# Optimization experiments

Measured on AMD Instinct MI355X. Metric: run time of the kernel, lower is better.

Reference implementation:

```python
import jax, jax.numpy as jnp
import numpy as np

B, S, IN, H, Q, M, K = 32, 2048, 128, 256, 16, 64, 3


def setup_inputs() -> dict:
    key = jax.random.key(0)
    ks = jax.random.split(key, 12)
    rn = lambda k, shp, s=0.05: (jax.random.normal(k, shp, jnp.float32) * s)
    return {
        "input_sequence": rn(ks[0], (B, S, IN), 1.0),
        "W_ih0": rn(ks[1], (4 * H, IN)),
        "W_hh0": rn(ks[2], (4 * H, H)),
        "b_ih0": jnp.zeros((4 * H,), jnp.float32),
        "b_hh0": jnp.zeros((4 * H,), jnp.float32),
        "W_ih1": rn(ks[3], (4 * H, H)),
        "W_hh1": rn(ks[4], (4 * H, H)),
        "b_ih1": jnp.zeros((4 * H,), jnp.float32),
        "b_hh1": jnp.zeros((4 * H,), jnp.float32),
        "W_cq": rn(ks[5], (Q, H)),
        "b_cq": jnp.zeros((Q,), jnp.float32),
        "mem_keys": rn(ks[6], (M, Q), 1.0),
        "mem_vals": rn(ks[7], (M, H), 1.0),
        "W_out": rn(ks[8], (H, 2 * H)),
        "b_out": jnp.zeros((H,), jnp.float32),
        "classical_weight": jnp.float32(0.7),
        "quantum_weight": jnp.float32(0.3),
    }


def _lstm_layer(x, W_ih, W_hh, b_ih, b_hh):
    """PyTorch-convention LSTM layer (gate order i,f,g,o), batch_first input."""
    Bb = x.shape[0]
    Hh = W_hh.shape[1]
    # precompute the input contribution for all timesteps: [B,S,4H]
    xg = jnp.einsum('bsi,gi->bsg', x, W_ih) + b_ih + b_hh

    def step(carry, xt):
        h, c = carry
        g = xt + h @ W_hh.T  # [B,4H]
        i, f, gg, o = jnp.split(g, 4, axis=-1)
        i = jax.nn.sigmoid(i)
        f = jax.nn.sigmoid(f)
        gg = jnp.tanh(gg)
        o = jax.nn.sigmoid(o)
        c = f * c + i * gg
        h = o * jnp.tanh(c)
        return (h, c), h

    init = (jnp.zeros((Bb, Hh), x.dtype), jnp.zeros((Bb, Hh), x.dtype))
    _, hs = jax.lax.scan(step, init, jnp.swapaxes(xg, 0, 1))  # [S,B,H]
    return jnp.swapaxes(hs, 0, 1)


def _forward(input_sequence, W_ih0, W_hh0, b_ih0, b_hh0, W_ih1, W_hh1, b_ih1,
             b_hh1, W_cq, b_cq, mem_keys, mem_vals, W_out, b_out,
             classical_weight, quantum_weight):
    # classical 2-layer LSTM
    h1 = _lstm_layer(input_sequence, W_ih0, W_hh0, b_ih0, b_hh0)
    lstm_out = _lstm_layer(h1, W_ih1, W_hh1, b_ih1, b_hh1)  # [B,S,H]

    # classical_to_quantum + tanh -> per-token query [B,S,Q]
    q = jnp.tanh(jnp.einsum('bsh,qh->bsq', lstm_out, W_cq) + b_cq)

    # batched k-NN read over the quantum memory (cosine similarity, k=3)
    eps = jnp.float32(1e-8)
    qn = q / (jnp.linalg.norm(q, axis=-1, keepdims=True) + eps)
    kn = mem_keys / (jnp.linalg.norm(mem_keys, axis=-1, keepdims=True) + eps)
    sims = jnp.einsum('bsq,mq->bsm', qn, kn)          # [B,S,M]
    top_vals, top_idx = jax.lax.top_k(sims, K)        # [B,S,K]
    gathered = mem_vals[top_idx]                      # [B,S,K,H]

    # similarity-weighted average of retrieved contents
    tot = jnp.sum(top_vals, axis=-1, keepdims=True)   # [B,S,1]
    weighted = jnp.einsum('bsk,bskh->bsh', top_vals, gathered)
    enhanced = jnp.where(tot > 0, weighted / jnp.where(tot == 0, 1.0, tot), 0.0)

    # combine streams and project
    combined = jnp.concatenate(
        [classical_weight * lstm_out, quantum_weight * enhanced], axis=-1)
    out = jnp.einsum('bsc,hc->bsh', combined, W_out) + b_out  # [B,S,H]
    return out


def reference(input_sequence, W_ih0, W_hh0, b_ih0, b_hh0, W_ih1, W_hh1, b_ih1,
              b_hh1, W_cq, b_cq, mem_keys, mem_vals, W_out, b_out,
              classical_weight, quantum_weight):
    return _forward(input_sequence, W_ih0, W_hh0, b_ih0, b_hh0, W_ih1, W_hh1,
                    b_ih1, b_hh1, W_cq, b_cq, mem_keys, mem_vals, W_out, b_out,
                    classical_weight, quantum_weight)
```

## Files before the change

kernel.cpp:

```cpp
#include <hip/hip_runtime.h>
#include <cstdint>
#include <cstddef>
#include <math.h>

#define B_   32
#define S_   2048
#define IN_  128
#define H_   256
#define Q_   16
#define M_   64
#define D_   4

typedef unsigned long long u64;
typedef __attribute__((ext_vector_type(4))) unsigned int u32x4;

__device__ __forceinline__ float4 ld4(const float* p) { return *(const float4*)p; }

#define AGLD64(p)    __hip_atomic_load((p),  __ATOMIC_RELAXED, __HIP_MEMORY_SCOPE_AGENT)
#define AGST64(p, v) __hip_atomic_store((p), (v), __ATOMIC_RELAXED, __HIP_MEMORY_SCOPE_AGENT)

__device__ __forceinline__ u32x4 mall_load_2x64(const u64* p) {
  u32x4 q;
  asm volatile("global_load_dwordx4 %0, %1, off sc0 sc1\n\ts_waitcnt vmcnt(0)"
               : "=v"(q) : "v"(p) : "memory");
  return q;
}

__device__ __forceinline__ float sigm_f(float x) { return 1.0f / (1.0f + __expf(-x)); }
__device__ __forceinline__ float tanh_f(float x) { return 1.0f - 2.0f / (__expf(2.0f * x) + 1.0f); }

__global__ __launch_bounds__(256, 1) void lstm2(
    const float* __restrict__ x,
    const float* __restrict__ Wih0, const float* __restrict__ bih0,
    const float* __restrict__ bhh0, const float* __restrict__ Whh0,
    const float* __restrict__ Wih1, const float* __restrict__ bih1,
    const float* __restrict__ bhh1, const float* __restrict__ Whh1,
    float* __restrict__ out,
    u64* __restrict__ exs)
{
  const int f = blockIdx.x;
  const int n = f >> 5;
  const int b = f & 31;

  const int tid = threadIdx.x;
  const int w   = tid >> 6;
  const int l   = tid & 63;
  const int kc  = l & 7;
  const int rg  = l >> 3;
  const int wrg = w * 8 + rg;
  const int col = n * 32 + wrg;

  __shared__ float w1[128][257];
  __shared__ float aring[8][256];
  __shared__ float hring[2][256];
  __shared__ float x_sh[2][IN_];

#pragma unroll
  for (int s2 = 0; s2 < 8; s2++) aring[s2][tid] = 0.0f;
  hring[0][tid] = 0.0f;
  hring[1][tid] = 0.0f;

  float4 wf0[4][8], wf1[4][8], wi0[4][4];
  float rb0[4], rb1[4];
#pragma unroll
  for (int g = 0; g < 4; g++) {
    const int row = g * 256 + col;
    const float* p0 = Whh0 + (size_t)row * 256 + 4 * kc;
    const float* p1 = Whh1 + (size_t)row * 256 + 4 * kc;
    const float* pi = Wih0 + (size_t)row * 128 + 4 * kc;
#pragma unroll
    for (int j = 0; j < 8; j++) {
      wf0[g][j] = ld4(p0 + 32 * j);
      wf1[g][j] = ld4(p1 + 32 * j);
    }
#pragma unroll
    for (int j = 0; j < 4; j++) wi0[g][j] = ld4(pi + 32 * j);
    rb0[g] = bih0[row] + bhh0[row];
    rb1[g] = bih1[row] + bhh1[row];
    const float* pw = Wih1 + (size_t)row * 256 + 4 * kc;
    float* dst = &w1[g * 32 + wrg][4 * kc];
#pragma unroll
    for (int j = 0; j < 8; j++) *(float4*)(dst + 32 * j) = ld4(pw + 32 * j);
  }

  const float* xrow = x + (size_t)b * S_ * IN_;
  float* outp = out + (size_t)b * S_ * H_;
  u64* sexb = exs + (size_t)b * 1024;

  if (tid < IN_) {
    x_sh[0][tid] = xrow[tid];
    x_sh[1][tid] = xrow[IN_ + tid];
  }
  float xreg = (tid < IN_) ? xrow[(size_t)2 * IN_ + tid] : 0.0f;
  float cst0 = 0.0f, cst1 = 0.0f;
  float xa0s[4], xa1s[4] = {0, 0, 0, 0};
  __syncthreads();

  {
    const float* xb = x_sh[0];
    float4 xv[4];
#pragma unroll
    for (int j = 0; j < 4; j++) xv[j] = ld4(xb + 4 * kc + 32 * j);
#pragma unroll
    for (int g = 0; g < 4; g++) {
      float4 s4 = {0, 0, 0, 0};
#pragma unroll
      for (int j = 0; j < 4; j++) {
        s4.x += wi0[g][j].x * xv[j].x; s4.y += wi0[g][j].y * xv[j].y;
        s4.z += wi0[g][j].z * xv[j].z; s4.w += wi0[g][j].w * xv[j].w;
      }
      float s = (s4.x + s4.y) + (s4.z + s4.w);
      s += __shfl_xor(s, 1); s += __shfl_xor(s, 2); s += __shfl_xor(s, 4);
      xa0s[g] = s + rb0[g];
    }
  }

  bool dead = false;
  for (int t = 0; t < S_ + D_; ++t) {
    const bool doA = (t < S_);
    const int  u   = t - D_;
    const bool doH = (u >= 0);
    const int  pa = t & 1, ph = u & 1;
    const unsigned eA = (unsigned)(t + 1), eH = (unsigned)(u + 1);

    float xreg_n = 0.0f;
    if (tid < IN_ && t + 2 < S_) {
      int tn = (t + 3 < S_) ? t + 3 : S_ - 1;
      xreg_n = xrow[(size_t)tn * IN_ + tid];
    }

    if (doA) {
      const float* ap = aring[(t - 1) & 7];
      float4 av[8];
#pragma unroll
      for (int j = 0; j < 8; j++) av[j] = ld4(ap + 4 * kc + 32 * j);
      float gv[4];
#pragma unroll
      for (int g = 0; g < 4; g++) {
        float4 s4 = {0, 0, 0, 0};
#pragma unroll
        for (int j = 0; j < 8; j++) {
          s4.x += wf0[g][j].x * av[j].x; s4.y += wf0[g][j].y * av[j].y;
          s4.z += wf0[g][j].z * av[j].z; s4.w += wf0[g][j].w * av[j].w;
        }
        float s = (s4.x + s4.y) + (s4.z + s4.w);
        s += __shfl_xor(s, 1); s += __shfl_xor(s, 2); s += __shfl_xor(s, 4);
        gv[g] = s + xa0s[g];
      }
      float ig = sigm_f(gv[0]);
      float fg = sigm_f(gv[1]);
      float cg = tanh_f(gv[2]);
      float og = sigm_f(gv[3]);
      cst0 = fg * cst0 + ig * cg;
      float a = og * tanh_f(cst0);
      if (kc == 0) {
        u64 pk = ((u64)eA << 32) | (u64)__float_as_uint(a);
        AGST64(sexb + ((0 * 2 + pa) << 8) + col, pk);
        aring[t & 7][col] = a;
      }
    }
    if (doH) {
      const float* hp = hring[(t - 1) & 1];
      float4 hv[8];
#pragma unroll
      for (int j = 0; j < 8; j++) hv[j] = ld4(hp + 4 * kc + 32 * j);
      float gv[4];
#pragma unroll
      for (int g = 0; g < 4; g++) {
        float4 s4 = {0, 0, 0, 0};
#pragma unroll
        for (int j = 0; j < 8; j++) {
          s4.x += wf1[g][j].x * hv[j].x; s4.y += wf1[g][j].y * hv[j].y;
          s4.z += wf1[g][j].z * hv[j].z; s4.w += wf1[g][j].w * hv[j].w;
        }
        float s = (s4.x + s4.y) + (s4.z + s4.w);
        s += __shfl_xor(s, 1); s += __shfl_xor(s, 2); s += __shfl_xor(s, 4);
        gv[g] = s + xa1s[g];
      }
      float ig = sigm_f(gv[0]);
      float fg = sigm_f(gv[1]);
      float cg = tanh_f(gv[2]);
      float og = sigm_f(gv[3]);
      cst1 = fg * cst1 + ig * cg;
      float h = og * tanh_f(cst1);
      if (kc == 0) {
        outp[(size_t)u * H_ + col] = h;
        u64 pk = ((u64)eH << 32) | (u64)__float_as_uint(h);
        AGST64(sexb + ((1 * 2 + ph) << 8) + col, pk);
        hring[u & 1][col] = h;
      }
    }

    if (t + 1 < S_) {
      const float* xb = x_sh[(t + 1) & 1];
      float4 xv[4];
#pragma unroll
      for (int j = 0; j < 4; j++) xv[j] = ld4(xb + 4 * kc + 32 * j);
#pragma unroll
      for (int g = 0; g < 4; g++) {
        float4 s4 = {0, 0, 0, 0};
#pragma unroll
        for (int j = 0; j < 4; j++) {
          s4.x += wi0[g][j].x * xv[j].x; s4.y += wi0[g][j].y * xv[j].y;
          s4.z += wi0[g][j].z * xv[j].z; s4.w += wi0[g][j].w * xv[j].w;
        }
        float s = (s4.x + s4.y) + (s4.z + s4.w);
        s += __shfl_xor(s, 1); s += __shfl_xor(s, 2); s += __shfl_xor(s, 4);
        xa0s[g] = s + rb0[g];
      }
    }
    {
      const int v = t - D_ + 1;
      if (v >= 0 && v < S_) {
        const float* avp = aring[v & 7];
        float4 av[8];
#pragma unroll
        for (int j = 0; j < 8; j++) av[j] = ld4(avp + 4 * kc + 32 * j);
#pragma unroll
        for (int g = 0; g < 4; g++) {
          const float* wr = &w1[g * 32 + wrg][4 * kc];
          float4 s4 = {0, 0, 0, 0};
#pragma unroll
          for (int j = 0; j < 8; j++) {
            float4 wv = ld4(wr + 32 * j);
            s4.x += wv.x * av[j].x; s4.y += wv.y * av[j].y;
            s4.z += wv.z * av[j].z; s4.w += wv.w * av[j].w;
          }
          float s = (s4.x + s4.y) + (s4.z + s4.w);
          s += __shfl_xor(s, 1); s += __shfl_xor(s, 2); s += __shfl_xor(s, 4);
          xa1s[g] = s + rb1[g];
        }
      }
    }

    {
      const bool isA = (tid < 128);
      const int  pi2 = isA ? tid : tid - 128;
      const bool ownp = ((pi2 >> 4) == n);
      const bool act  = isA ? doA : doH;
      bool need = act && !ownp && !dead;
      if (need) {
        const unsigned etag = isA ? eA : eH;
        const int plane = isA ? (0 * 2 + pa) : (1 * 2 + ph);
        u64* base = sexb + (plane << 8) + 2 * pi2;
        unsigned val0 = 0, val1 = 0;
        bool got = false;
#pragma unroll 1
        for (int it = 0; it < 16 && !got; ++it) {
          u32x4 q = mall_load_2x64(base);
          if (q.y == etag && q.w == etag) { val0 = q.x; val1 = q.z; got = true; }
        }
        if (!got) {
          bool g0 = false, g1 = false;
          unsigned guard = 0;
          while (!(g0 && g1)) {
            if (!g0) { u64 v = AGLD64(base);     if ((unsigned)(v >> 32) == etag) { val0 = (unsigned)v; g0 = true; } }
            if (!g1) { u64 v = AGLD64(base + 1); if ((unsigned)(v >> 32) == etag) { val1 = (unsigned)v; g1 = true; } }
            if (++guard >= (1u << 20)) { dead = true; break; }
          }
        }
        float2 f2;
        f2.x = __uint_as_float(val0);
        f2.y = __uint_as_float(val1);
        if (isA) *(float2*)&aring[t & 7][2 * pi2] = f2;
        else     *(float2*)&hring[u & 1][2 * pi2] = f2;
      }
    }

    if (tid < IN_ && t < S_) x_sh[t & 1][tid] = xreg;
    xreg = xreg_n;
    __syncthreads();
  }
}

__global__ __launch_bounds__(256) void knn_enh(
    const float* __restrict__ lstm, const float* __restrict__ Wcq,
    const float* __restrict__ bcq, const float* __restrict__ keys,
    const float* __restrict__ vals, const float* __restrict__ qwp,
    float* __restrict__ enh)
{
  const int tid  = threadIdx.x;
  const int wave = tid >> 6, lane = tid & 63;
  const int t = blockIdx.x * 4 + wave;

  __shared__ float xsh[4][256];
  __shared__ float qsh[4][16];

  const float* xrow = lstm + (size_t)t * H_;
  float4 x4 = ld4(xrow + lane * 4);
  *(float4*)&xsh[wave][lane * 4] = x4;
  __syncthreads();

  const int j = lane & 15, seg = lane >> 4;
  const float* wrow = Wcq + j * H_ + seg * 64;
  const float* xseg = &xsh[wave][seg * 64];
  float p = 0.0f;
#pragma unroll
  for (int c = 0; c < 64; c += 4) {
    float4 w4 = ld4(wrow + c);
    p += w4.x * xseg[c] + w4.y * xseg[c + 1] + w4.z * xseg[c + 2] + w4.w * xseg[c + 3];
  }
  p += __shfl_xor(p, 16);
  p += __shfl_xor(p, 32);
  float q = tanhf(p + bcq[j]);

  float sq = q * q;
  sq += __shfl_xor(sq, 1); sq += __shfl_xor(sq, 2);
  sq += __shfl_xor(sq, 4); sq += __shfl_xor(sq, 8);
  float qn = q / (sqrtf(sq) + 1e-8f);
  if (lane < 16) qsh[wave][lane] = qn;
  __syncthreads();

  const int m = lane;
  const float* krow = keys + m * Q_;
  float kv[16]; float kn2 = 0.0f;
#pragma unroll
  for (int jj = 0; jj < 16; jj++) { kv[jj] = krow[jj]; kn2 += kv[jj] * kv[jj]; }
  float rn = 1.0f / (sqrtf(kn2) + 1e-8f);
  float sim = 0.0f;
#pragma unroll
  for (int jj = 0; jj < 16; jj++) sim += qsh[wave][jj] * kv[jj];
  sim *= rn;

  float rem = sim;
  float tv[3]; int ti[3];
#pragma unroll
  for (int k = 0; k < 3; k++) {
    float v = rem; int idx = m;
#pragma unroll
    for (int d = 1; d < 64; d <<= 1) {
      float ov = __shfl_xor(v, d);
      int   oi = __shfl_xor(idx, d);
      if (ov > v || (ov == v && oi < idx)) { v = ov; idx = oi; }
    }
    tv[k] = v; ti[k] = idx;
    if (m == idx) rem = -INFINITY;
  }
  float tot = tv[0] + tv[1] + tv[2];

  float ex = 0, ey = 0, ez = 0, ew = 0;
#pragma unroll
  for (int k = 0; k < 3; k++) {
    float4 vv = ld4(vals + (size_t)ti[k] * H_ + lane * 4);
    ex += tv[k] * vv.x; ey += tv[k] * vv.y;
    ez += tv[k] * vv.z; ew += tv[k] * vv.w;
  }
  float inv = (tot > 0.0f) ? 1.0f / tot : 0.0f;
  const float qw = qwp[0];

  float4 o;
  o.x = qw * ex * inv; o.y = qw * ey * inv;
  o.z = qw * ez * inv; o.w = qw * ew * inv;
  *(float4*)&enh[(size_t)t * H_ + lane * 4] = o;
}

__global__ __launch_bounds__(256) void gemm_cat(
    float* __restrict__ io, const float* __restrict__ A2,
    const float* __restrict__ Bw, const float* __restrict__ bias,
    const float* __restrict__ cwp)
{
  __shared__ float As[16][68];
  __shared__ float Bs[16][260];
  const int tid  = threadIdx.x;
  const int row0 = blockIdx.x * 64;
  const int tx = tid & 15, ty = tid >> 4;
  const int lr = tid >> 2;
  const int lk = (tid & 3) << 2;
  const float cw = cwp[0];

  float acc[4][16];
#pragma unroll
  for (int i = 0; i < 4; i++)
#pragma unroll
    for (int j = 0; j < 16; j++) acc[i][j] = 0.0f;

  for (int k0 = 0; k0 < 512; k0 += 16) {
    float4 av;
    if (k0 < 256) {
      av = ld4(io + (size_t)(row0 + lr) * 256 + k0 + lk);
      av.x *= cw; av.y *= cw; av.z *= cw; av.w *= cw;
    } else {
      av = ld4(A2 + (size_t)(row0 + lr) * 256 + (k0 - 256) + lk);
    }
    As[lk + 0][lr] = av.x; As[lk + 1][lr] = av.y;
    As[lk + 2][lr] = av.z; As[lk + 3][lr] = av.w;
    const float* bp = Bw + (size_t)tid * 512 + k0;
#pragma unroll
    for (int q = 0; q < 4; q++) {
      float4 b4 = ld4(bp + 4 * q);
      Bs[4 * q + 0][tid] = b4.x; Bs[4 * q + 1][tid] = b4.y;
      Bs[4 * q + 2][tid] = b4.z; Bs[4 * q + 3][tid] = b4.w;
    }
    __syncthreads();
#pragma unroll
    for (int k = 0; k < 16; k++) {
      float4 a4 = *(const float4*)&As[k][ty << 2];
      float aa[4] = {a4.x, a4.y, a4.z, a4.w};
#pragma unroll
      for (int cc = 0; cc < 4; cc++) {
        float4 b4 = *(const float4*)&Bs[k][cc * 64 + (tx << 2)];
        float bb[4] = {b4.x, b4.y, b4.z, b4.w};
#pragma unroll
        for (int i = 0; i < 4; i++)
#pragma unroll
          for (int jj = 0; jj < 4; jj++) acc[i][cc * 4 + jj] += aa[i] * bb[jj];
      }
    }
    __syncthreads();
  }

#pragma unroll
  for (int i = 0; i < 4; i++) {
#pragma unroll
    for (int cc = 0; cc < 4; cc++) {
      int c0 = cc * 64 + (tx << 2);
      float4 o;
      o.x = acc[i][cc * 4 + 0] + bias[c0 + 0];
      o.y = acc[i][cc * 4 + 1] + bias[c0 + 1];
      o.z = acc[i][cc * 4 + 2] + bias[c0 + 2];
      o.w = acc[i][cc * 4 + 3] + bias[c0 + 3];
      *(float4*)&io[(size_t)(row0 + (ty << 2) + i) * 256 + c0] = o;
    }
  }
}

extern "C" void kernel_launch(void* const* d_in, const int* in_sizes, int n_in,
                              void* d_out, int out_size, void* d_ws, size_t ws_size,
                              hipStream_t stream)
{
  const float* x    = (const float*)d_in[0];
  const float* Wih0 = (const float*)d_in[1];
  const float* Whh0 = (const float*)d_in[2];
  const float* bih0 = (const float*)d_in[3];
  const float* bhh0 = (const float*)d_in[4];
  const float* Wih1 = (const float*)d_in[5];
  const float* Whh1 = (const float*)d_in[6];
  const float* bih1 = (const float*)d_in[7];
  const float* bhh1 = (const float*)d_in[8];
  const float* Wcq  = (const float*)d_in[9];
  const float* bcq  = (const float*)d_in[10];
  const float* keys = (const float*)d_in[11];
  const float* vals = (const float*)d_in[12];
  const float* Wout = (const float*)d_in[13];
  const float* bout = (const float*)d_in[14];
  const float* cw   = (const float*)d_in[15];
  const float* qw   = (const float*)d_in[16];
  float* out = (float*)d_out;

  const size_t HE = (size_t)B_ * S_ * H_;
  if (ws_size < HE * sizeof(float)) return;
  u64* exs = (u64*)d_ws;
  float* enh = (float*)d_ws;

  const int MT = B_ * S_;
  dim3 blk(256);

  hipMemsetAsync(exs, 0, (size_t)32 * 1024 * sizeof(u64), stream);
  lstm2<<<dim3(256), blk, 0, stream>>>(x, Wih0, bih0, bhh0, Whh0,
                                       Wih1, bih1, bhh1, Whh1, out, exs);

  knn_enh<<<dim3(MT / 4), blk, 0, stream>>>(out, Wcq, bcq, keys, vals, qw, enh);

  gemm_cat<<<dim3(MT / 64), blk, 0, stream>>>(out, enh, Wout, bout, cw);
}
```

Measured before the change: 13.57 ms.

## Process four batch rows per LSTM block and batch cross-block exchange loads

Each persistent LSTM block now handles four batch rows for its 32-column slice, which cuts the grid from 256 to 64 blocks. The register-resident weights are reused across the rows, and the four rows' peer-exchange polls are issued together as one batched set of MALL loads. The aim is to amortise per-step synchronisation and exchange latency over more work per step. In exchange, each block does roughly four times the serial compute per timestep, so per-step latency may rise. Register pressure also grows with the per-row state arrays.

Result: slower. 33.91 ms (+149.9%).

```diff
diff --git a/kernel.cpp b/kernel.cpp
--- a/kernel.cpp
+++ b/kernel.cpp
@@ -10,6 +10,7 @@
 #define Q_   16
 #define M_   64
 #define D_   4
+#define R_   4
 
 typedef unsigned long long u64;
 typedef __attribute__((ext_vector_type(4))) unsigned int u32x4;
@@ -24,6 +25,20 @@
   asm volatile("global_load_dwordx4 %0, %1, off sc0 sc1\n\ts_waitcnt vmcnt(0)"
                : "=v"(q) : "v"(p) : "memory");
   return q;
+}
+__device__ __forceinline__ void mall_load4(const u64* p0, const u64* p1,
+                                           const u64* p2, const u64* p3,
+                                           u32x4& q0, u32x4& q1,
+                                           u32x4& q2, u32x4& q3) {
+  asm volatile(
+      "global_load_dwordx4 %0, %4, off sc0 sc1\n\t"
+      "global_load_dwordx4 %1, %5, off sc0 sc1\n\t"
+      "global_load_dwordx4 %2, %6, off sc0 sc1\n\t"
+      "global_load_dwordx4 %3, %7, off sc0 sc1\n\t"
+      "s_waitcnt vmcnt(0)"
+      : "=&v"(q0), "=&v"(q1), "=&v"(q2), "=&v"(q3)
+      : "v"(p0), "v"(p1), "v"(p2), "v"(p3)
+      : "memory");
 }
 
 __device__ __forceinline__ float sigm_f(float x) { return 1.0f / (1.0f + __expf(-x)); }
@@ -38,9 +53,9 @@
     float* __restrict__ out,
     u64* __restrict__ exs)
 {
-  const int f = blockIdx.x;
-  const int n = f >> 5;
-  const int b = f & 31;
+  const int f  = blockIdx.x;
+  const int n  = f & 7;
+  const int r0 = (f >> 3) * R_;
 
   const int tid = threadIdx.x;
   const int w   = tid >> 6;
@@ -51,14 +66,12 @@
   const int col = n * 32 + wrg;
 
   __shared__ float w1[128][257];
-  __shared__ float aring[8][256];
-  __shared__ float hring[2][256];
-  __shared__ float x_sh[2][IN_];
-
-#pragma unroll
-  for (int s2 = 0; s2 < 8; s2++) aring[s2][tid] = 0.0f;
-  hring[0][tid] = 0.0f;
-  hring[1][tid] = 0.0f;
+  __shared__ float aring[4][R_][256];
+  __shared__ float hring[2][R_][256];
+  __shared__ float x_sh[2][R_][IN_];
+
+  for (int i = tid; i < 4 * R_ * 256; i += 256) ((float*)aring)[i] = 0.0f;
+  for (int i = tid; i < 2 * R_ * 256; i += 256) ((float*)hring)[i] = 0.0f;
 
   float4 wf0[4][8], wf1[4][8], wi0[4][4];
   float rb0[4], rb1[4];
@@ -83,21 +96,25 @@
     for (int j = 0; j < 8; j++) *(float4*)(dst + 32 * j) = ld4(pw + 32 * j);
   }
 
-  const float* xrow = x + (size_t)b * S_ * IN_;
-  float* outp = out + (size_t)b * S_ * H_;
-  u64* sexb = exs + (size_t)b * 1024;
-
-  if (tid < IN_) {
-    x_sh[0][tid] = xrow[tid];
-    x_sh[1][tid] = xrow[IN_ + tid];
-  }
-  float xreg = (tid < IN_) ? xrow[(size_t)2 * IN_ + tid] : 0.0f;
-  float cst0 = 0.0f, cst1 = 0.0f;
-  float xa0s[4], xa1s[4] = {0, 0, 0, 0};
+  const int xrr = tid >> 6, xe = (tid & 63) * 2;
+  const float* xrow_t = x + (size_t)(r0 + xrr) * S_ * IN_ + xe;
+  *(float2*)&x_sh[0][xrr][xe] = *(const float2*)(xrow_t);
+  *(float2*)&x_sh[1][xrr][xe] = *(const float2*)(xrow_t + IN_);
+  float2 xreg = *(const float2*)(xrow_t + 2 * IN_);
+
+  float cst0[R_], cst1[R_];
+  float xa0s[R_][4], xa1s[R_][4];
+#pragma unroll
+  for (int rr = 0; rr < R_; rr++) {
+    cst0[rr] = 0.0f; cst1[rr] = 0.0f;
+#pragma unroll
+    for (int g = 0; g < 4; g++) xa1s[rr][g] = 0.0f;
+  }
   __syncthreads();
 
-  {
-    const float* xb = x_sh[0];
+#pragma unroll
+  for (int rr = 0; rr < R_; rr++) {
+    const float* xb = x_sh[0][rr];
     float4 xv[4];
 #pragma unroll
     for (int j = 0; j < 4; j++) xv[j] = ld4(xb + 4 * kc + 32 * j);
@@ -111,7 +128,7 @@
       }
       float s = (s4.x + s4.y) + (s4.z + s4.w);
       s += __shfl_xor(s, 1); s += __shfl_xor(s, 2); s += __shfl_xor(s, 4);
-      xa0s[g] = s + rb0[g];
+      xa0s[rr][g] = s + rb0[g];
     }
   }
 
@@ -123,151 +140,173 @@
     const int  pa = t & 1, ph = u & 1;
     const unsigned eA = (unsigned)(t + 1), eH = (unsigned)(u + 1);
 
-    float xreg_n = 0.0f;
-    if (tid < IN_ && t + 2 < S_) {
+    float2 xreg_n = {0.0f, 0.0f};
+    if (t + 2 < S_) {
       int tn = (t + 3 < S_) ? t + 3 : S_ - 1;
-      xreg_n = xrow[(size_t)tn * IN_ + tid];
+      xreg_n = *(const float2*)(xrow_t + (size_t)tn * IN_);
     }
 
     if (doA) {
-      const float* ap = aring[(t - 1) & 7];
-      float4 av[8];
-#pragma unroll
-      for (int j = 0; j < 8; j++) av[j] = ld4(ap + 4 * kc + 32 * j);
-      float gv[4];
-#pragma unroll
-      for (int g = 0; g < 4; g++) {
-        float4 s4 = {0, 0, 0, 0};
-#pragma unroll
-        for (int j = 0; j < 8; j++) {
-          s4.x += wf0[g][j].x * av[j].x; s4.y += wf0[g][j].y * av[j].y;
-          s4.z += wf0[g][j].z * av[j].z; s4.w += wf0[g][j].w * av[j].w;
-        }
-        float s = (s4.x + s4.y) + (s4.z + s4.w);
-        s += __shfl_xor(s, 1); s += __shfl_xor(s, 2); s += __shfl_xor(s, 4);
-        gv[g] = s + xa0s[g];
-      }
-      float ig = sigm_f(gv[0]);
-      float fg = sigm_f(gv[1]);
-      float cg = tanh_f(gv[2]);
-      float og = sigm_f(gv[3]);
-      cst0 = fg * cst0 + ig * cg;
-      float a = og * tanh_f(cst0);
-      if (kc == 0) {
-        u64 pk = ((u64)eA << 32) | (u64)__float_as_uint(a);
-        AGST64(sexb + ((0 * 2 + pa) << 8) + col, pk);
-        aring[t & 7][col] = a;
+#pragma unroll
+      for (int rr = 0; rr < R_; rr++) {
+        const float* ap = aring[(t - 1) & 3][rr];
+        float4 av[8];
+#pragma unroll
+        for (int j = 0; j < 8; j++) av[j] = ld4(ap + 4 * kc + 32 * j);
+        float gv[4];
+#pragma unroll
+        for (int g = 0; g < 4; g++) {
+          float4 s4 = {0, 0, 0, 0};
+#pragma unroll
+          for (int j = 0; j < 8; j++) {
+            s4.x += wf0[g][j].x * av[j].x; s4.y += wf0[g][j].y * av[j].y;
+            s4.z += wf0[g][j].z * av[j].z; s4.w += wf0[g][j].w * av[j].w;
+          }
+          float s = (s4.x + s4.y) + (s4.z + s4.w);
+          s += __shfl_xor(s, 1); s += __shfl_xor(s, 2); s += __shfl_xor(s, 4);
+          gv[g] = s + xa0s[rr][g];
+        }
+        float ig = sigm_f(gv[0]);
+        float fg = sigm_f(gv[1]);
+        float cg = tanh_f(gv[2]);
+        float og = sigm_f(gv[3]);
+        cst0[rr] = fg * cst0[rr] + ig * cg;
+        float a = og * tanh_f(cst0[rr]);
+        if (kc == 0) {
+          u64 pk = ((u64)eA << 32) | (u64)__float_as_uint(a);
+          AGST64(exs + (size_t)(r0 + rr) * 1024 + ((0 * 2 + pa) << 8) + col, pk);
+          aring[t & 3][rr][col] = a;
+        }
       }
     }
     if (doH) {
-      const float* hp = hring[(t - 1) & 1];
-      float4 hv[8];
-#pragma unroll
-      for (int j = 0; j < 8; j++) hv[j] = ld4(hp + 4 * kc + 32 * j);
-      float gv[4];
-#pragma unroll
-      for (int g = 0; g < 4; g++) {
-        float4 s4 = {0, 0, 0, 0};
-#pragma unroll
-        for (int j = 0; j < 8; j++) {
-          s4.x += wf1[g][j].x * hv[j].x; s4.y += wf1[g][j].y * hv[j].y;
-          s4.z += wf1[g][j].z * hv[j].z; s4.w += wf1[g][j].w * hv[j].w;
-        }
-        float s = (s4.x + s4.y) + (s4.z + s4.w);
-        s += __shfl_xor(s, 1); s += __shfl_xor(s, 2); s += __shfl_xor(s, 4);
-        gv[g] = s + xa1s[g];
-      }
-      float ig = sigm_f(gv[0]);
-      float fg = sigm_f(gv[1]);
-      float cg = tanh_f(gv[2]);
-      float og = sigm_f(gv[3]);
-      cst1 = fg * cst1 + ig * cg;
-      float h = og * tanh_f(cst1);
-      if (kc == 0) {
-        outp[(size_t)u * H_ + col] = h;
-        u64 pk = ((u64)eH << 32) | (u64)__float_as_uint(h);
-        AGST64(sexb + ((1 * 2 + ph) << 8) + col, pk);
-        hring[u & 1][col] = h;
+#pragma unroll
+      for (int rr = 0; rr < R_; rr++) {
+        const float* hp = hring[(t - 1) & 1][rr];
+        float4 hv[8];
+#pragma unroll
+        for (int j = 0; j < 8; j++) hv[j] = ld4(hp + 4 * kc + 32 * j);
+        float gv[4];
+#pragma unroll
+        for (int g = 0; g < 4; g++) {
+          float4 s4 = {0, 0, 0, 0};
+#pragma unroll
+          for (int j = 0; j < 8; j++) {
+            s4.x += wf1[g][j].x * hv[j].x; s4.y += wf1[g][j].y * hv[j].y;
+            s4.z += wf1[g][j].z * hv[j].z; s4.w += wf1[g][j].w * hv[j].w;
+          }
+          float s = (s4.x + s4.y) + (s4.z + s4.w);
+          s += __shfl_xor(s, 1); s += __shfl_xor(s, 2); s += __shfl_xor(s, 4);
+          gv[g] = s + xa1s[rr][g];
+        }
+        float ig = sigm_f(gv[0]);
+        float fg = sigm_f(gv[1]);
+        float cg = tanh_f(gv[2]);
+        float og = sigm_f(gv[3]);
+        cst1[rr] = fg * cst1[rr] + ig * cg;
+        float h = og * tanh_f(cst1[rr]);
+        if (kc == 0) {
+          u64 pk = ((u64)eH << 32) | (u64)__float_as_uint(h);
+          AGST64(exs + (size_t)(r0 + rr) * 1024 + ((1 * 2 + ph) << 8) + col, pk);
+          out[((size_t)(r0 + rr) * S_ + u) * H_ + col] = h;
+          hring[u & 1][rr][col] = h;
+        }
       }
     }
 
     if (t + 1 < S_) {
-      const float* xb = x_sh[(t + 1) & 1];
-      float4 xv[4];
-#pragma unroll
-      for (int j = 0; j < 4; j++) xv[j] = ld4(xb + 4 * kc + 32 * j);
-#pragma unroll
-      for (int g = 0; g < 4; g++) {
-        float4 s4 = {0, 0, 0, 0};
-#pragma unroll
-        for (int j = 0; j < 4; j++) {
-          s4.x += wi0[g][j].x * xv[j].x; s4.y += wi0[g][j].y * xv[j].y;
-          s4.z += wi0[g][j].z * xv[j].z; s4.w += wi0[g][j].w * xv[j].w;
-        }
-        float s = (s4.x + s4.y) + (s4.z + s4.w);
-        s += __shfl_xor(s, 1); s += __shfl_xor(s, 2); s += __shfl_xor(s, 4);
-        xa0s[g] = s + rb0[g];
+#pragma unroll
+      for (int rr = 0; rr < R_; rr++) {
+        const float* xb = x_sh[(t + 1) & 1][rr];
+        float4 xv[4];
+#pragma unroll
+        for (int j = 0; j < 4; j++) xv[j] = ld4(xb + 4 * kc + 32 * j);
+#pragma unroll
+        for (int g = 0; g < 4; g++) {
+          float4 s4 = {0, 0, 0, 0};
+#pragma unroll
+          for (int j = 0; j < 4; j++) {
+            s4.x += wi0[g][j].x * xv[j].x; s4.y += wi0[g][j].y * xv[j].y;
+            s4.z += wi0[g][j].z * xv[j].z; s4.w += wi0[g][j].w * xv[j].w;
+          }
+          float s = (s4.x + s4.y) + (s4.z + s4.w);
+          s += __shfl_xor(s, 1); s += __shfl_xor(s, 2); s += __shfl_xor(s, 4);
+          xa0s[rr][g] = s + rb0[g];
+        }
       }
     }
     {
       const int v = t - D_ + 1;
       if (v >= 0 && v < S_) {
-        const float* avp = aring[v & 7];
-        float4 av[8];
-#pragma unroll
-        for (int j = 0; j < 8; j++) av[j] = ld4(avp + 4 * kc + 32 * j);
-#pragma unroll
-        for (int g = 0; g < 4; g++) {
-          const float* wr = &w1[g * 32 + wrg][4 * kc];
-          float4 s4 = {0, 0, 0, 0};
-#pragma unroll
-          for (int j = 0; j < 8; j++) {
-            float4 wv = ld4(wr + 32 * j);
-            s4.x += wv.x * av[j].x; s4.y += wv.y * av[j].y;
-            s4.z += wv.z * av[j].z; s4.w += wv.w * av[j].w;
+#pragma unroll
+        for (int rr = 0; rr < R_; rr++) {
+          const float* avp = aring[v & 3][rr];
+          float4 av[8];
+#pragma unroll
+          for (int j = 0; j < 8; j++) av[j] = ld4(avp + 4 * kc + 32 * j);
+#pragma unroll
+          for (int g = 0; g < 4; g++) {
+            const float* wr = &w1[g * 32 + wrg][4 * kc];
+            float4 s4 = {0, 0, 0, 0};
+#pragma unroll
+            for (int j = 0; j < 8; j++) {
+              float4 wv = ld4(wr + 32 * j);
+              s4.x += wv.x * av[j].x; s4.y += wv.y * av[j].y;
+              s4.z += wv.z * av[j].z; s4.w += wv.w * av[j].w;
+            }
+            float s = (s4.x + s4.y) + (s4.z + s4.w);
+            s += __shfl_xor(s, 1); s += __shfl_xor(s, 2); s += __shfl_xor(s, 4);
+            xa1s[rr][g] = s + rb1[g];
           }
-          float s = (s4.x + s4.y) + (s4.z + s4.w);
-          s += __shfl_xor(s, 1); s += __shfl_xor(s, 2); s += __shfl_xor(s, 4);
-          xa1s[g] = s + rb1[g];
         }
       }
     }
 
     {
       const bool isA = (tid < 128);
-      const int  pi2 = isA ? tid : tid - 128;
+      const int  pi2 = tid & 127;
       const bool ownp = ((pi2 >> 4) == n);
       const bool act  = isA ? doA : doH;
-      bool need = act && !ownp && !dead;
-      if (need) {
+      if (act && !ownp && !dead) {
         const unsigned etag = isA ? eA : eH;
         const int plane = isA ? (0 * 2 + pa) : (1 * 2 + ph);
-        u64* base = sexb + (plane << 8) + 2 * pi2;
-        unsigned val0 = 0, val1 = 0;
-        bool got = false;
+        u64* base0 = exs + (size_t)(r0 + 0) * 1024 + (plane << 8) + 2 * pi2;
+        u64* base1 = base0 + 1024;
+        u64* base2 = base0 + 2048;
+        u64* base3 = base0 + 3072;
+        u32x4 q0, q1, q2, q3;
+        mall_load4(base0, base1, base2, base3, q0, q1, q2, q3);
+        u32x4 qs[R_] = {q0, q1, q2, q3};
+        u64* bases[R_] = {base0, base1, base2, base3};
+#pragma unroll
+        for (int rr = 0; rr < R_; rr++) {
+          u32x4 q = qs[rr];
+          bool got = (q.y == etag && q.w == etag);
 #pragma unroll 1
-        for (int it = 0; it < 16 && !got; ++it) {
-          u32x4 q = mall_load_2x64(base);
-          if (q.y == etag && q.w == etag) { val0 = q.x; val1 = q.z; got = true; }
-        }
-        if (!got) {
-          bool g0 = false, g1 = false;
-          unsigned guard = 0;
-          while (!(g0 && g1)) {
-            if (!g0) { u64 v = AGLD64(base);     if ((unsigned)(v >> 32) == etag) { val0 = (unsigned)v; g0 = true; } }
-            if (!g1) { u64 v = AGLD64(base + 1); if ((unsigned)(v >> 32) == etag) { val1 = (unsigned)v; g1 = true; } }
-            if (++guard >= (1u << 20)) { dead = true; break; }
+          for (int it = 0; it < 16 && !got; ++it) {
+            q = mall_load_2x64(bases[rr]);
+            got = (q.y == etag && q.w == etag);
           }
-        }
-        float2 f2;
-        f2.x = __uint_as_float(val0);
-        f2.y = __uint_as_float(val1);
-        if (isA) *(float2*)&aring[t & 7][2 * pi2] = f2;
-        else     *(float2*)&hring[u & 1][2 * pi2] = f2;
-      }
-    }
-
-    if (tid < IN_ && t < S_) x_sh[t & 1][tid] = xreg;
+          unsigned val0 = q.x, val1 = q.z;
+          if (!got) {
+            bool g0 = false, g1 = false;
+            unsigned guard = 0;
+            while (!(g0 && g1)) {
+              if (!g0) { u64 v2 = AGLD64(bases[rr]);     if ((unsigned)(v2 >> 32) == etag) { val0 = (unsigned)v2; g0 = true; } }
+              if (!g1) { u64 v2 = AGLD64(bases[rr] + 1); if ((unsigned)(v2 >> 32) == etag) { val1 = (unsigned)v2; g1 = true; } }
+              if (++guard >= (1u << 20)) { dead = true; break; }
+            }
+          }
+          float2 f2;
+          f2.x = __uint_as_float(val0);
+          f2.y = __uint_as_float(val1);
+          if (isA) *(float2*)&aring[t & 3][rr][2 * pi2] = f2;
+          else     *(float2*)&hring[u & 1][rr][2 * pi2] = f2;
+        }
+      }
+    }
+
+    if (t < S_) *(float2*)&x_sh[t & 1][xrr][xe] = xreg;
     xreg = xreg_n;
     __syncthreads();
   }
@@ -456,8 +495,8 @@
   dim3 blk(256);
 
   hipMemsetAsync(exs, 0, (size_t)32 * 1024 * sizeof(u64), stream);
-  lstm2<<<dim3(256), blk, 0, stream>>>(x, Wih0, bih0, bhh0, Whh0,
-                                       Wih1, bih1, bhh1, Whh1, out, exs);
+  lstm2<<<dim3(64), blk, 0, stream>>>(x, Wih0, bih0, bhh0, Whh0,
+                                      Wih1, bih1, bhh1, Whh1, out, exs);
 
   knn_enh<<<dim3(MT / 4), blk, 0, stream>>>(out, Wcq, bcq, keys, vals, qw, enh);
 
```

## Process two batch rows per LSTM block, halving grid and overlapping exchange loads

Applied to the files above, without the earlier changes.

Each persistent LSTM block now handles two batch rows instead of one, so the register-resident recurrent weights are reused across rows and the grid shrinks from 256 to 128 blocks. The cross-block exchange now issues both rows' MALL loads before the input-projection work and waits on them afterwards, hiding part of the polling latency. The aring ring is reduced to 4 slots per row to fit the extra LDS. The trade-off is roughly double the serial compute per block per timestep, which may lengthen the critical path of the recurrence.

New measurement: 23.44 ms. +72.7%, slower.

```diff
diff --git a/kernel.cpp b/kernel.cpp
--- a/kernel.cpp
+++ b/kernel.cpp
@@ -10,6 +10,7 @@
 #define Q_   16
 #define M_   64
 #define D_   4
+#define R_   2
 
 typedef unsigned long long u64;
 typedef __attribute__((ext_vector_type(4))) unsigned int u32x4;
@@ -24,6 +25,15 @@
   asm volatile("global_load_dwordx4 %0, %1, off sc0 sc1\n\ts_waitcnt vmcnt(0)"
                : "=v"(q) : "v"(p) : "memory");
   return q;
+}
+__device__ __forceinline__ void mall_issue2(const u64* p0, const u64* p1,
+                                            u32x4& q0, u32x4& q1) {
+  asm volatile("global_load_dwordx4 %0, %2, off sc0 sc1\n\t"
+               "global_load_dwordx4 %1, %3, off sc0 sc1"
+               : "=&v"(q0), "=&v"(q1) : "v"(p0), "v"(p1) : "memory");
+}
+__device__ __forceinline__ void mall_wait2(u32x4& q0, u32x4& q1) {
+  asm volatile("s_waitcnt vmcnt(0)" : "+v"(q0), "+v"(q1) :: "memory");
 }
 
 __device__ __forceinline__ float sigm_f(float x) { return 1.0f / (1.0f + __expf(-x)); }
@@ -38,9 +48,9 @@
     float* __restrict__ out,
     u64* __restrict__ exs)
 {
-  const int f = blockIdx.x;
-  const int n = f >> 5;
-  const int b = f & 31;
+  const int f  = blockIdx.x;
+  const int n  = f & 7;
+  const int r0 = (f >> 3) * R_;
 
   const int tid = threadIdx.x;
   const int w   = tid >> 6;
@@ -51,14 +61,12 @@
   const int col = n * 32 + wrg;
 
   __shared__ float w1[128][257];
-  __shared__ float aring[8][256];
-  __shared__ float hring[2][256];
-  __shared__ float x_sh[2][IN_];
-
-#pragma unroll
-  for (int s2 = 0; s2 < 8; s2++) aring[s2][tid] = 0.0f;
-  hring[0][tid] = 0.0f;
-  hring[1][tid] = 0.0f;
+  __shared__ float aring[4][R_][256];
+  __shared__ float hring[2][R_][256];
+  __shared__ float x_sh[2][R_][IN_];
+
+  for (int i = tid; i < 4 * R_ * 256; i += 256) ((float*)aring)[i] = 0.0f;
+  for (int i = tid; i < 2 * R_ * 256; i += 256) ((float*)hring)[i] = 0.0f;
 
   float4 wf0[4][8], wf1[4][8], wi0[4][4];
   float rb0[4], rb1[4];
@@ -83,37 +91,96 @@
     for (int j = 0; j < 8; j++) *(float4*)(dst + 32 * j) = ld4(pw + 32 * j);
   }
 
-  const float* xrow = x + (size_t)b * S_ * IN_;
-  float* outp = out + (size_t)b * S_ * H_;
-  u64* sexb = exs + (size_t)b * 1024;
-
-  if (tid < IN_) {
-    x_sh[0][tid] = xrow[tid];
-    x_sh[1][tid] = xrow[IN_ + tid];
-  }
-  float xreg = (tid < IN_) ? xrow[(size_t)2 * IN_ + tid] : 0.0f;
-  float cst0 = 0.0f, cst1 = 0.0f;
-  float xa0s[4], xa1s[4] = {0, 0, 0, 0};
+  const int xrr = tid >> 7, xe = tid & 127;
+  const float* xrow_t = x + (size_t)(r0 + xrr) * S_ * IN_ + xe;
+  x_sh[0][xrr][xe] = xrow_t[0];
+  x_sh[1][xrr][xe] = xrow_t[IN_];
+  float xreg = xrow_t[2 * IN_];
+
+  float cst0_0 = 0.0f, cst0_1 = 0.0f, cst1_0 = 0.0f, cst1_1 = 0.0f;
+  float xa0s_0[4], xa0s_1[4];
+  float xa1s_0[4] = {0, 0, 0, 0}, xa1s_1[4] = {0, 0, 0, 0};
   __syncthreads();
 
-  {
-    const float* xb = x_sh[0];
-    float4 xv[4];
-#pragma unroll
-    for (int j = 0; j < 4; j++) xv[j] = ld4(xb + 4 * kc + 32 * j);
-#pragma unroll
-    for (int g = 0; g < 4; g++) {
-      float4 s4 = {0, 0, 0, 0};
-#pragma unroll
-      for (int j = 0; j < 4; j++) {
-        s4.x += wi0[g][j].x * xv[j].x; s4.y += wi0[g][j].y * xv[j].y;
-        s4.z += wi0[g][j].z * xv[j].z; s4.w += wi0[g][j].w * xv[j].w;
-      }
-      float s = (s4.x + s4.y) + (s4.z + s4.w);
-      s += __shfl_xor(s, 1); s += __shfl_xor(s, 2); s += __shfl_xor(s, 4);
-      xa0s[g] = s + rb0[g];
-    }
-  }
+#define XA0_ROW(RR, BUF)                                                     \
+  { const float* xb = x_sh[BUF][RR];                                         \
+    float4 xv[4];                                                            \
+    _Pragma("unroll") for (int j = 0; j < 4; j++)                            \
+      xv[j] = ld4(xb + 4 * kc + 32 * j);                                     \
+    _Pragma("unroll") for (int g = 0; g < 4; g++) {                          \
+      float4 s4 = {0, 0, 0, 0};                                              \
+      _Pragma("unroll") for (int j = 0; j < 4; j++) {                        \
+        s4.x += wi0[g][j].x * xv[j].x; s4.y += wi0[g][j].y * xv[j].y;        \
+        s4.z += wi0[g][j].z * xv[j].z; s4.w += wi0[g][j].w * xv[j].w; }      \
+      float s = (s4.x + s4.y) + (s4.z + s4.w);                               \
+      s += __shfl_xor(s, 1); s += __shfl_xor(s, 2); s += __shfl_xor(s, 4);   \
+      xa0s_##RR[g] = s + rb0[g]; } }
+
+#define L0_ROW(RR)                                                           \
+  { const float* ap = aring[(t - 1) & 3][RR];                                \
+    float4 av[8];                                                            \
+    _Pragma("unroll") for (int j = 0; j < 8; j++)                            \
+      av[j] = ld4(ap + 4 * kc + 32 * j);                                     \
+    float gv[4];                                                             \
+    _Pragma("unroll") for (int g = 0; g < 4; g++) {                          \
+      float4 s4 = {0, 0, 0, 0};                                              \
+      _Pragma("unroll") for (int j = 0; j < 8; j++) {                        \
+        s4.x += wf0[g][j].x * av[j].x; s4.y += wf0[g][j].y * av[j].y;        \
+        s4.z += wf0[g][j].z * av[j].z; s4.w += wf0[g][j].w * av[j].w; }      \
+      float s = (s4.x + s4.y) + (s4.z + s4.w);                               \
+      s += __shfl_xor(s, 1); s += __shfl_xor(s, 2); s += __shfl_xor(s, 4);   \
+      gv[g] = s + xa0s_##RR[g]; }                                            \
+    float ig = sigm_f(gv[0]), fg = sigm_f(gv[1]);                            \
+    float cg = tanh_f(gv[2]), og = sigm_f(gv[3]);                            \
+    cst0_##RR = fg * cst0_##RR + ig * cg;                                    \
+    float a = og * tanh_f(cst0_##RR);                                        \
+    if (kc == 0) {                                                           \
+      u64 pk = ((u64)eA << 32) | (u64)__float_as_uint(a);                    \
+      AGST64(exs + (size_t)(r0 + RR) * 1024 + (pa << 8) + col, pk);          \
+      aring[t & 3][RR][col] = a; } }
+
+#define L1_ROW(RR)                                                           \
+  { const float* hp = hring[(t - 1) & 1][RR];                                \
+    float4 hv[8];                                                            \
+    _Pragma("unroll") for (int j = 0; j < 8; j++)                            \
+      hv[j] = ld4(hp + 4 * kc + 32 * j);                                     \
+    float gv[4];                                                             \
+    _Pragma("unroll") for (int g = 0; g < 4; g++) {                          \
+      float4 s4 = {0, 0, 0, 0};                                              \
+      _Pragma("unroll") for (int j = 0; j < 8; j++) {                        \
+        s4.x += wf1[g][j].x * hv[j].x; s4.y += wf1[g][j].y * hv[j].y;        \
+        s4.z += wf1[g][j].z * hv[j].z; s4.w += wf1[g][j].w * hv[j].w; }      \
+      float s = (s4.x + s4.y) + (s4.z + s4.w);                               \
+      s += __shfl_xor(s, 1); s += __shfl_xor(s, 2); s += __shfl_xor(s, 4);   \
+      gv[g] = s + xa1s_##RR[g]; }                                            \
+    float ig = sigm_f(gv[0]), fg = sigm_f(gv[1]);                            \
+    float cg = tanh_f(gv[2]), og = sigm_f(gv[3]);                            \
+    cst1_##RR = fg * cst1_##RR + ig * cg;                                    \
+    float h = og * tanh_f(cst1_##RR);                                        \
+    if (kc == 0) {                                                           \
+      u64 pk = ((u64)eH << 32) | (u64)__float_as_uint(h);                    \
+      AGST64(exs + (size_t)(r0 + RR) * 1024 + ((2 + ph) << 8) + col, pk);    \
+      out[((size_t)(r0 + RR) * S_ + u) * H_ + col] = h;                      \
+      hring[u & 1][RR][col] = h; } }
+
+#define XA1_ROW(RR)                                                          \
+  { const float* avp = aring[v & 3][RR];                                     \
+    float4 av[8];                                                            \
+    _Pragma("unroll") for (int j = 0; j < 8; j++)                            \
+      av[j] = ld4(avp + 4 * kc + 32 * j);                                    \
+    _Pragma("unroll") for (int g = 0; g < 4; g++) {                          \
+      const float* wr = &w1[g * 32 + wrg][4 * kc];                           \
+      float4 s4 = {0, 0, 0, 0};                                              \
+      _Pragma("unroll") for (int j = 0; j < 8; j++) {                        \
+        float4 wv = ld4(wr + 32 * j);                                        \
+        s4.x += wv.x * av[j].x; s4.y += wv.y * av[j].y;                      \
+        s4.z += wv.z * av[j].z; s4.w += wv.w * av[j].w; }                    \
+      float s = (s4.x + s4.y) + (s4.z + s4.w);                               \
+      s += __shfl_xor(s, 1); s += __shfl_xor(s, 2); s += __shfl_xor(s, 4);   \
+      xa1s_##RR[g] = s + rb1[g]; } }
+
+  XA0_ROW(0, 0)
+  XA0_ROW(1, 0)
 
   bool dead = false;
   for (int t = 0; t < S_ + D_; ++t) {
@@ -124,153 +191,83 @@
     const unsigned eA = (unsigned)(t + 1), eH = (unsigned)(u + 1);
 
     float xreg_n = 0.0f;
-    if (tid < IN_ && t + 2 < S_) {
+    if (t + 2 < S_) {
       int tn = (t + 3 < S_) ? t + 3 : S_ - 1;
-      xreg_n = xrow[(size_t)tn * IN_ + tid];
-    }
-
-    if (doA) {
-      const float* ap = aring[(t - 1) & 7];
-      float4 av[8];
-#pragma unroll
-      for (int j = 0; j < 8; j++) av[j] = ld4(ap + 4 * kc + 32 * j);
-      float gv[4];
-#pragma unroll
-      for (int g = 0; g < 4; g++) {
-        float4 s4 = {0, 0, 0, 0};
-#pragma unroll
-        for (int j = 0; j < 8; j++) {
-          s4.x += wf0[g][j].x * av[j].x; s4.y += wf0[g][j].y * av[j].y;
-          s4.z += wf0[g][j].z * av[j].z; s4.w += wf0[g][j].w * av[j].w;
-        }
-        float s = (s4.x + s4.y) + (s4.z + s4.w);
-        s += __shfl_xor(s, 1); s += __shfl_xor(s, 2); s += __shfl_xor(s, 4);
-        gv[g] = s + xa0s[g];
-      }
-      float ig = sigm_f(gv[0]);
-      float fg = sigm_f(gv[1]);
-      float cg = tanh_f(gv[2]);
-      float og = sigm_f(gv[3]);
-      cst0 = fg * cst0 + ig * cg;
-      float a = og * tanh_f(cst0);
-      if (kc == 0) {
-        u64 pk = ((u64)eA << 32) | (u64)__float_as_uint(a);
-        AGST64(sexb + ((0 * 2 + pa) << 8) + col, pk);
-        aring[t & 7][col] = a;
-      }
-    }
-    if (doH) {
-      const float* hp = hring[(t - 1) & 1];
-      float4 hv[8];
-#pragma unroll
-      for (int j = 0; j < 8; j++) hv[j] = ld4(hp + 4 * kc + 32 * j);
-      float gv[4];
-#pragma unroll
-      for (int g = 0; g < 4; g++) {
-        float4 s4 = {0, 0, 0, 0};
-#pragma unroll
-        for (int j = 0; j < 8; j++) {
-          s4.x += wf1[g][j].x * hv[j].x; s4.y += wf1[g][j].y * hv[j].y;
-          s4.z += wf1[g][j].z * hv[j].z; s4.w += wf1[g][j].w * hv[j].w;
-        }
-        float s = (s4.x + s4.y) + (s4.z + s4.w);
-        s += __shfl_xor(s, 1); s += __shfl_xor(s, 2); s += __shfl_xor(s, 4);
-        gv[g] = s + xa1s[g];
-      }
-      float ig = sigm_f(gv[0]);
-      float fg = sigm_f(gv[1]);
-      float cg = tanh_f(gv[2]);
-      float og = sigm_f(gv[3]);
-      cst1 = fg * cst1 + ig * cg;
-      float h = og * tanh_f(cst1);
-      if (kc == 0) {
-        outp[(size_t)u * H_ + col] = h;
-        u64 pk = ((u64)eH << 32) | (u64)__float_as_uint(h);
-        AGST64(sexb + ((1 * 2 + ph) << 8) + col, pk);
-        hring[u & 1][col] = h;
-      }
-    }
+      xreg_n = xrow_t[(size_t)tn * IN_];
+    }
+
+    if (doA) { L0_ROW(0) L0_ROW(1) }
+    if (doH) { L1_ROW(0) L1_ROW(1) }
+
+    const bool isA = (tid < 128);
+    const int  pi2 = tid & 127;
+    const bool ownp = ((pi2 >> 4) == n);
+    const bool act  = isA ? doA : doH;
+    const bool need = act && !ownp && !dead;
+    const unsigned etag = isA ? eA : eH;
+    const int plane = isA ? pa : 2 + ph;
+    u64* b0 = exs + (size_t)(r0 + 0) * 1024 + (plane << 8) + 2 * pi2;
+    u64* b1 = b0 + 1024;
+    u32x4 q0, q1;
+    if (need) mall_issue2(b0, b1, q0, q1);
 
     if (t + 1 < S_) {
-      const float* xb = x_sh[(t + 1) & 1];
-      float4 xv[4];
-#pragma unroll
-      for (int j = 0; j < 4; j++) xv[j] = ld4(xb + 4 * kc + 32 * j);
-#pragma unroll
-      for (int g = 0; g < 4; g++) {
-        float4 s4 = {0, 0, 0, 0};
-#pragma unroll
-        for (int j = 0; j < 4; j++) {
-          s4.x += wi0[g][j].x * xv[j].x; s4.y += wi0[g][j].y * xv[j].y;
-          s4.z += wi0[g][j].z * xv[j].z; s4.w += wi0[g][j].w * xv[j].w;
-        }
-        float s = (s4.x + s4.y) + (s4.z + s4.w);
-        s += __shfl_xor(s, 1); s += __shfl_xor(s, 2); s += __shfl_xor(s, 4);
-        xa0s[g] = s + rb0[g];
-      }
+      const int nb = (t + 1) & 1;
+      XA0_ROW(0, nb)
+      XA0_ROW(1, nb)
     }
     {
       const int v = t - D_ + 1;
-      if (v >= 0 && v < S_) {
-        const float* avp = aring[v & 7];
-        float4 av[8];
-#pragma unroll
-        for (int j = 0; j < 8; j++) av[j] = ld4(avp + 4 * kc + 32 * j);
-#pragma unroll
-        for (int g = 0; g < 4; g++) {
-          const float* wr = &w1[g * 32 + wrg][4 * kc];
-          float4 s4 = {0, 0, 0, 0};
-#pragma unroll
-          for (int j = 0; j < 8; j++) {
-            float4 wv = ld4(wr + 32 * j);
-            s4.x += wv.x * av[j].x; s4.y += wv.y * av[j].y;
-            s4.z += wv.z * av[j].z; s4.w += wv.w * av[j].w;
+      if (v >= 0 && v < S_) { XA1_ROW(0) XA1_ROW(1) }
+    }
+
+    if (need) {
+      mall_wait2(q0, q1);
+      bool got0 = (q0.y == etag && q0.w == etag);
+      bool got1 = (q1.y == etag && q1.w == etag);
+#pragma unroll 1
+      for (int it = 0; it < 16 && !(got0 && got1); ++it) {
+        if (!got0) { q0 = mall_load_2x64(b0); got0 = (q0.y == etag && q0.w == etag); }
+        if (!got1) { q1 = mall_load_2x64(b1); got1 = (q1.y == etag && q1.w == etag); }
+      }
+      if (!(got0 && got1)) {
+        unsigned guard = 0;
+        while (!(got0 && got1)) {
+          if (!got0) {
+            u64 va = AGLD64(b0), vb = AGLD64(b0 + 1);
+            if ((unsigned)(va >> 32) == etag && (unsigned)(vb >> 32) == etag) {
+              q0.x = (unsigned)va; q0.z = (unsigned)vb; got0 = true;
+            }
           }
-          float s = (s4.x + s4.y) + (s4.z + s4.w);
-          s += __shfl_xor(s, 1); s += __shfl_xor(s, 2); s += __shfl_xor(s, 4);
-          xa1s[g] = s + rb1[g];
+          if (!got1) {
+            u64 va = AGLD64(b1), vb = AGLD64(b1 + 1);
+            if ((unsigned)(va >> 32) == etag && (unsigned)(vb >> 32) == etag) {
+              q1.x = (unsigned)va; q1.z = (unsigned)vb; got1 = true;
+            }
+          }
+          if (++guard >= (1u << 20)) { dead = true; break; }
         }
       }
-    }
-
-    {
-      const bool isA = (tid < 128);
-      const int  pi2 = isA ? tid : tid - 128;
-      const bool ownp = ((pi2 >> 4) == n);
-      const bool act  = isA ? doA : doH;
-      bool need = act && !ownp && !dead;
-      if (need) {
-        const unsigned etag = isA ? eA : eH;
-        const int plane = isA ? (0 * 2 + pa) : (1 * 2 + ph);
-        u64* base = sexb + (plane << 8) + 2 * pi2;
-        unsigned val0 = 0, val1 = 0;
-        bool got = false;
-#pragma unroll 1
-        for (int it = 0; it < 16 && !got; ++it) {
-          u32x4 q = mall_load_2x64(base);
-          if (q.y == etag && q.w == etag) { val0 = q.x; val1 = q.z; got = true; }
-        }
-        if (!got) {
-          bool g0 = false, g1 = false;
-          unsigned guard = 0;
-          while (!(g0 && g1)) {
-            if (!g0) { u64 v = AGLD64(base);     if ((unsigned)(v >> 32) == etag) { val0 = (unsigned)v; g0 = true; } }
-            if (!g1) { u64 v = AGLD64(base + 1); if ((unsigned)(v >> 32) == etag) { val1 = (unsigned)v; g1 = true; } }
-            if (++guard >= (1u << 20)) { dead = true; break; }
-          }
-        }
-        float2 f2;
-        f2.x = __uint_as_float(val0);
-        f2.y = __uint_as_float(val1);
-        if (isA) *(float2*)&aring[t & 7][2 * pi2] = f2;
-        else     *(float2*)&hring[u & 1][2 * pi2] = f2;
+      float2 f0, f1;
+      f0.x = __uint_as_float(q0.x); f0.y = __uint_as_float(q0.z);
+      f1.x = __uint_as_float(q1.x); f1.y = __uint_as_float(q1.z);
+      if (isA) {
+        *(float2*)&aring[t & 3][0][2 * pi2] = f0;
+        *(float2*)&aring[t & 3][1][2 * pi2] = f1;
+      } else {
+        *(float2*)&hring[u & 1][0][2 * pi2] = f0;
+        *(float2*)&hring[u & 1][1][2 * pi2] = f1;
       }
     }
 
-    if (tid < IN_ && t < S_) x_sh[t & 1][tid] = xreg;
+    if (t < S_) x_sh[t & 1][xrr][xe] = xreg;
     xreg = xreg_n;
     __syncthreads();
   }
+#undef XA0_ROW
+#undef L0_ROW
+#undef L1_ROW
+#undef XA1_ROW
 }
 
 __global__ __launch_bounds__(256) void knn_enh(
@@ -456,7 +453,7 @@
   dim3 blk(256);
 
   hipMemsetAsync(exs, 0, (size_t)32 * 1024 * sizeof(u64), stream);
-  lstm2<<<dim3(256), blk, 0, stream>>>(x, Wih0, bih0, bhh0, Whh0,
+  lstm2<<<dim3(128), blk, 0, stream>>>(x, Wih0, bih0, bhh0, Whh0,
                                        Wih1, bih1, bhh1, Whh1, out, exs);
 
   knn_enh<<<dim3(MT / 4), blk, 0, stream>>>(out, Wcq, bcq, keys, vals, qw, enh);
```
